# Optimization experiments

Hardware: AMD Instinct MI355X
Metric: run time of the kernel (lower is better)

Reference implementation:

```python
import jax, jax.numpy as jnp
import numpy as np

NUM_STATES = 512
NUM_OBS = 1024
BATCH = 64
T = 512


def setup_inputs() -> dict:
    key = jax.random.key(0)
    k_obs, k_pi, k_A, k_B = jax.random.split(key, 4)
    observations = jax.random.randint(k_obs, (BATCH, T), 0, NUM_OBS, dtype=jnp.int32)
    log_pi = jax.random.normal(k_pi, (NUM_STATES,), dtype=jnp.float32)
    log_A = jax.random.normal(k_A, (NUM_STATES, NUM_STATES), dtype=jnp.float32)
    log_B = jax.random.normal(k_B, (NUM_STATES, NUM_OBS), dtype=jnp.float32)
    return {"observations": observations, "log_pi": log_pi, "log_A": log_A, "log_B": log_B}


def _hmm_loglik(observations, log_pi, log_A, log_B):
    # Normalize parameters in log-space (as in the torch module).
    lpi = jax.nn.log_softmax(log_pi, axis=0)            # (S,)
    lA = jax.nn.log_softmax(log_A, axis=1)              # (S, S)
    lB = jax.nn.log_softmax(log_B, axis=1)              # (S, O)

    # Emission log-probs per timestep: (B, T, S)
    emit = lB.T[observations]                            # gather columns of lB

    alpha0 = lpi[None, :] + emit[:, 0, :]                # (B, S)

    def step(alpha, emit_t):
        # alpha: (B, S) over previous state i; transition lA[i, j]
        alpha_next = jax.scipy.special.logsumexp(alpha[:, :, None] + lA[None, :, :], axis=1) + emit_t
        return alpha_next, None

    # scan over time axis; emit[:, 1:, :] -> (T-1, B, S)
    alpha_T, _ = jax.lax.scan(step, alpha0, jnp.swapaxes(emit[:, 1:, :], 0, 1))
    log_probs = jax.scipy.special.logsumexp(alpha_T, axis=1)  # (B,)
    return log_probs.sum()


def reference(observations, log_pi, log_A, log_B):
    return _hmm_loglik(observations, log_pi, log_A, log_B)
```

## Files before the change

### kernel.cpp

```cpp
#include <hip/hip_runtime.h>

#define S     512
#define NOBS  1024
#define TT    512
#define CH    16
#define NWAVE 8
#define NJT   4
#define NGRP  4

typedef __attribute__((ext_vector_type(4))) float f32x4;
typedef __attribute__((ext_vector_type(4))) int   i32x4;
typedef __attribute__((ext_vector_type(8))) int   i32x8;
typedef __attribute__((ext_vector_type(2))) unsigned int u32x2;
typedef long i64;

__device__ __forceinline__ unsigned short f2bf(float x) {
  unsigned u = __builtin_bit_cast(unsigned, x);
  return (unsigned short)((u + 0x7fffu + ((u >> 16) & 1u)) >> 16);
}
__device__ __forceinline__ float bflo(unsigned u) {
  return __builtin_bit_cast(float, u << 16);
}
__device__ __forceinline__ float bfhi(unsigned u) {
  return __builtin_bit_cast(float, u & 0xffff0000u);
}

__device__ __forceinline__ unsigned char f2fp8_sw(float x) {
  x = fminf(fmaxf(x, 0.f), 448.f);
  unsigned u = __builtin_bit_cast(unsigned, x);
  int ex = (int)((u >> 23) & 0xff);
  if (ex >= 121) {
    unsigned m = (u & 0x7fffff) | 0x800000;
    unsigned keep = m >> 20, rest = m & 0xfffff;
    keep += (rest > 0x80000u) || (rest == 0x80000u && (keep & 1));
    int e8 = ex - 127 + 7;
    if (keep == 16) { keep = 8; e8++; }
    if (e8 >= 16) return 0x7e;
    return (unsigned char)((e8 << 3) | (keep & 7));
  } else {
    int m = (int)(x * 512.0f + 0.5f);
    if (m > 8) m = 8;
    return (unsigned char)m;
  }
}

__device__ __forceinline__ unsigned pack4_fp8(float p0, float p1, float p2, float p3) {
#if __has_builtin(__builtin_amdgcn_cvt_pk_fp8_f32)
  int v = __builtin_amdgcn_cvt_pk_fp8_f32(p0, p1, 0, false);
  v = __builtin_amdgcn_cvt_pk_fp8_f32(p2, p3, v, true);
  return (unsigned)v;
#else
  return (unsigned)f2fp8_sw(p0) | ((unsigned)f2fp8_sw(p1) << 8) |
         ((unsigned)f2fp8_sw(p2) << 16) | ((unsigned)f2fp8_sw(p3) << 24);
#endif
}

__device__ __forceinline__ float wave_max(float v) {
  for (int d = 32; d; d >>= 1) v = fmaxf(v, __shfl_xor(v, d));
  return v;
}
__device__ __forceinline__ float wave_sum(float v) {
  for (int d = 32; d; d >>= 1) v += __shfl_xor(v, d);
  return v;
}

__global__ void prep_pi(const float* __restrict__ log_pi, float* __restrict__ lpi) {
  const int l = threadIdx.x;
  float v[8];
  float mx = -INFINITY;
  for (int k = 0; k < 8; ++k) { v[k] = log_pi[l + 64 * k]; mx = fmaxf(mx, v[k]); }
  mx = wave_max(mx);
  float sm = 0.f;
  for (int k = 0; k < 8; ++k) sm += __expf(v[k] - mx);
  sm = wave_sum(sm);
  const float lse = mx + __logf(sm);
  for (int k = 0; k < 8; ++k) lpi[l + 64 * k] = v[k] - lse;
}

__global__ void prep_B(const float* __restrict__ log_B, unsigned short* __restrict__ Bexp16) {
  const int j = blockIdx.x, l = threadIdx.x;
  const float* row = log_B + (size_t)j * NOBS;
  float v[16];
  float mx = -INFINITY;
  for (int k = 0; k < 16; ++k) { v[k] = row[l + 64 * k]; mx = fmaxf(mx, v[k]); }
  mx = wave_max(mx);
  float sm = 0.f;
  for (int k = 0; k < 16; ++k) sm += __expf(v[k] - mx);
  sm = wave_sum(sm);
  const float lse = mx + __logf(sm);
  for (int k = 0; k < 16; ++k) Bexp16[(size_t)(l + 64 * k) * S + j] = f2bf(__expf(v[k] - lse));
}

__global__ void prep_A(const float* __restrict__ log_A, unsigned char* __restrict__ Afrag8) {
  const int i = blockIdx.x, l = threadIdx.x;
  const float* row = log_A + (size_t)i * S;
  float v[8];
  float mx = -INFINITY;
  for (int k = 0; k < 8; ++k) { v[k] = row[l + 64 * k]; mx = fmaxf(mx, v[k]); }
  mx = wave_max(mx);
  float sm = 0.f;
  for (int k = 0; k < 8; ++k) sm += __expf(v[k] - mx);
  sm = wave_sum(sm);
  const float lse = mx + __logf(sm);
  const int c = i >> 7, g4s = (i >> 5) & 3, e = i & 31;
  for (int k = 0; k < 8; ++k) {
    const int j = l + 64 * k;
    const int jt = j >> 4, jc = j & 15;
    Afrag8[((size_t)(jt * 4 + c) * 64 + g4s * 16 + jc) * 32 + e] = f2fp8_sw(__expf(v[k] - lse));
  }
}

__device__ __forceinline__ int pswz(int m, int g) { return m * 512 + (((g ^ m) & 31) << 4); }

__global__ __launch_bounds__(512, 2)
void hmm_main(const int* __restrict__ obs, const float* __restrict__ lpi,
              const unsigned short* __restrict__ Bexp16,
              const unsigned char* __restrict__ Afrag8, float* __restrict__ parts)
{
  __shared__ __align__(16) unsigned char Pb[CH * S];
  __shared__ int   obs_s[CH][TT];
  __shared__ __align__(16) float pred[CH][NWAVE];

  const int tid = threadIdx.x;
  const int w   = tid >> 6;
  const int l   = tid & 63;
  const int g4  = l >> 4;
  const int mm  = l & 15;
  const int grp = blockIdx.x;

  i32x8 a_frags[NJT][4];
  #pragma unroll
  for (int ji = 0; ji < NJT; ++ji) {
    const int jt = w + NWAVE * ji;
    #pragma unroll
    for (int c = 0; c < 4; ++c)
      a_frags[ji][c] = *reinterpret_cast<const i32x8*>(
          Afrag8 + ((size_t)(jt * 4 + c) * 64 + l) * 32);
  }

  for (int m = 0; m < CH; ++m)
    obs_s[m][tid] = obs[(size_t)(grp * CH + m) * TT + tid];
  __syncthreads();

  float lsc = 0.f;

  for (int t = 0; t < TT; ++t) {
    const bool fin = (t == TT - 1);
    f32x4 vals[NJT];

    if (t == 0) {
      const int o0 = obs_s[mm][0];
      #pragma unroll
      for (int ji = 0; ji < NJT; ++ji) {
        const int j0 = (w + NWAVE * ji) * 16 + g4 * 4;
        const f32x4 lp = *reinterpret_cast<const f32x4*>(lpi + j0);
        const u32x2 e = *reinterpret_cast<const u32x2*>(Bexp16 + (size_t)o0 * S + j0);
        vals[ji][0] = lp[0] + __logf(bflo(e[0]));
        vals[ji][1] = lp[1] + __logf(bfhi(e[0]));
        vals[ji][2] = lp[2] + __logf(bflo(e[1]));
        vals[ji][3] = lp[3] + __logf(bfhi(e[1]));
      }
    } else {
      const int ob = obs_s[mm][t];
      u32x2 eb[NJT];
      const unsigned short* bp = Bexp16 + (size_t)ob * S + g4 * 4;
      #pragma unroll
      for (int ji = 0; ji < NJT; ++ji)
        eb[ji] = *reinterpret_cast<const u32x2*>(bp + (w + NWAVE * ji) * 16);

      i32x8 af[4];
      #pragma unroll
      for (int c = 0; c < 4; ++c) {
        const int g0 = c * 8 + g4 * 2;
        i32x4 lo = *reinterpret_cast<const i32x4*>(&Pb[pswz(mm, g0)]);
        i32x4 hi = *reinterpret_cast<const i32x4*>(&Pb[pswz(mm, g0 + 1)]);
        af[c] = i32x8{lo[0], lo[1], lo[2], lo[3], hi[0], hi[1], hi[2], hi[3]};
      }
      #pragma unroll
      for (int ji = 0; ji < NJT; ++ji) {
        f32x4 acc = {0.f, 0.f, 0.f, 0.f};
        #pragma unroll
        for (int c = 0; c < 4; ++c) {
#if __has_builtin(__builtin_amdgcn_mfma_scale_f32_16x16x128_f8f6f4)
          acc = __builtin_amdgcn_mfma_scale_f32_16x16x128_f8f6f4(
                    a_frags[ji][c], af[c], acc, 0, 0,
                    0, 0x7f7f7f7f, 0, 0x7f7f7f7f);
#else
          const i64* pa = reinterpret_cast<const i64*>(&a_frags[ji][c]);
          const i64* pb = reinterpret_cast<const i64*>(&af[c]);
          #pragma unroll
          for (int q = 0; q < 4; ++q)
            acc = __builtin_amdgcn_mfma_f32_16x16x32_fp8_fp8(pa[q], pb[q], acc, 0, 0, 0);
#endif
        }
        acc[0] *= bflo(eb[ji][0]);
        acc[1] *= bfhi(eb[ji][0]);
        acc[2] *= bflo(eb[ji][1]);
        acc[3] *= bfhi(eb[ji][1]);
        vals[ji] = acc;
      }
    }

    float v;
    if (fin) {
      f32x4 sv = vals[0] + vals[1] + vals[2] + vals[3];
      v = (sv[0] + sv[1]) + (sv[2] + sv[3]);
      v += __shfl_xor(v, 16);
      v += __shfl_xor(v, 32);
    } else {
      f32x4 mv;
      #pragma unroll
      for (int r = 0; r < 4; ++r)
        mv[r] = fmaxf(fmaxf(vals[0][r], vals[1][r]), fmaxf(vals[2][r], vals[3][r]));
      v = fmaxf(fmaxf(mv[0], mv[1]), fmaxf(mv[2], mv[3]));
      v = fmaxf(v, __shfl_xor(v, 16));
      v = fmaxf(v, __shfl_xor(v, 32));
    }
    if (g4 == 0) pred[mm][w] = v;
    __syncthreads();

    if (!fin) {
      const f32x4 p0 = *reinterpret_cast<const f32x4*>(&pred[mm][0]);
      const f32x4 p1 = *reinterpret_cast<const f32x4*>(&pred[mm][4]);
      const float s = fmaxf(fmaxf(fmaxf(p0[0], p0[1]), fmaxf(p0[2], p0[3])),
                            fmaxf(fmaxf(p1[0], p1[1]), fmaxf(p1[2], p1[3])));
      float inv;
      if (t == 0) { lsc = s;           inv = s; }
      else        { lsc += __logf(s);  inv = __builtin_amdgcn_rcpf(s); }

      #pragma unroll
      for (int ji = 0; ji < NJT; ++ji) {
        const int jt = w + NWAVE * ji;
        float q0, q1, q2, q3;
        if (t == 0) {
          q0 = __expf(vals[ji][0] - inv); q1 = __expf(vals[ji][1] - inv);
          q2 = __expf(vals[ji][2] - inv); q3 = __expf(vals[ji][3] - inv);
        } else {
          q0 = vals[ji][0] * inv; q1 = vals[ji][1] * inv;
          q2 = vals[ji][2] * inv; q3 = vals[ji][3] * inv;
        }
        *reinterpret_cast<unsigned*>(&Pb[pswz(mm, jt) + g4 * 4]) = pack4_fp8(q0, q1, q2, q3);
      }
      __syncthreads();
    } else {
      if (w == 0 && g4 == 0) {
        const f32x4 p0 = *reinterpret_cast<const f32x4*>(&pred[mm][0]);
        const f32x4 p1 = *reinterpret_cast<const f32x4*>(&pred[mm][4]);
        const float s8 = ((p0[0] + p0[1]) + (p0[2] + p0[3])) +
                         ((p1[0] + p1[1]) + (p1[2] + p1[3]));
        float cl = lsc + __logf(s8);
        for (int d = 1; d < 16; d <<= 1) cl += __shfl_xor(cl, d);
        if (l == 0) parts[grp] = cl;
      }
    }
  }
}

__global__ void final_sum(const float* __restrict__ parts, float* __restrict__ out) {
  out[0] = parts[0] + parts[1] + parts[2] + parts[3];
}

extern "C" void kernel_launch(void* const* d_in, const int* in_sizes, int n_in,
                              void* d_out, int out_size, void* d_ws, size_t ws_size,
                              hipStream_t stream) {
  const int*   obs  = (const int*)d_in[0];
  const float* lgpi = (const float*)d_in[1];
  const float* lgA  = (const float*)d_in[2];
  const float* lgB  = (const float*)d_in[3];
  float* out = (float*)d_out;

  char* ws = (char*)d_ws;
  unsigned short* Bexp16 = (unsigned short*)ws;
  unsigned char*  Afrag8 = (unsigned char*)(ws + (size_t)NOBS * S * 2);
  float*          lpi    = (float*)(ws + (size_t)NOBS * S * 2 + (size_t)S * S);
  float*          parts  = lpi + S;

  prep_pi<<<1, 64, 0, stream>>>(lgpi, lpi);
  prep_B<<<S, 64, 0, stream>>>(lgB, Bexp16);
  prep_A<<<S, 64, 0, stream>>>(lgA, Afrag8);
  hmm_main<<<NGRP, 512, 0, stream>>>(obs, lpi, Bexp16, Afrag8, parts);
  final_sum<<<1, 1, 0, stream>>>(parts, out);
}
```

Baseline: 841.6 us.

## Double-buffer probability tile and use predicted scale to drop one barrier per step

The per-step loop now uses double-buffered shared-memory probability and max buffers. The normalization scale for step t is predicted from the previous step's max plus a clamped growth-rate extrapolation, so the MFMA results can be scaled and written straight to the next buffer. This cuts the block barriers per timestep from two to one and removes the separate max-then-normalize pass from the critical path. In exchange, values can drift away from unit max within the clamped range, which may cost some FP8 precision.

```diff
diff --git a/kernel.cpp b/kernel.cpp
--- a/kernel.cpp
+++ b/kernel.cpp
@@ -112,20 +112,31 @@
 
 __device__ __forceinline__ int pswz(int m, int g) { return m * 512 + (((g ^ m) & 31) << 4); }
 
+__device__ __forceinline__ float max8(const float* p) {
+  const f32x4 p0 = *reinterpret_cast<const f32x4*>(p);
+  const f32x4 p1 = *reinterpret_cast<const f32x4*>(p + 4);
+  return fmaxf(fmaxf(fmaxf(p0[0], p0[1]), fmaxf(p0[2], p0[3])),
+               fmaxf(fmaxf(p1[0], p1[1]), fmaxf(p1[2], p1[3])));
+}
+__device__ __forceinline__ float sum8(const float* p) {
+  const f32x4 p0 = *reinterpret_cast<const f32x4*>(p);
+  const f32x4 p1 = *reinterpret_cast<const f32x4*>(p + 4);
+  return ((p0[0] + p0[1]) + (p0[2] + p0[3])) + ((p1[0] + p1[1]) + (p1[2] + p1[3]));
+}
+
+#define CLAMP_LN8 2.0794415f
+
 __global__ __launch_bounds__(512, 2)
 void hmm_main(const int* __restrict__ obs, const float* __restrict__ lpi,
               const unsigned short* __restrict__ Bexp16,
               const unsigned char* __restrict__ Afrag8, float* __restrict__ parts)
 {
-  __shared__ __align__(16) unsigned char Pb[CH * S];
-  __shared__ int   obs_s[CH][TT];
-  __shared__ __align__(16) float pred[CH][NWAVE];
+  __shared__ __align__(16) unsigned char Pb[2][CH * S];
+  __shared__ int obs_s[CH][TT + 1];
+  __shared__ __align__(16) float pred[2][CH][12];
 
   const int tid = threadIdx.x;
-  const int w   = tid >> 6;
-  const int l   = tid & 63;
-  const int g4  = l >> 4;
-  const int mm  = l & 15;
+  const int w = tid >> 6, l = tid & 63, g4 = l >> 4, mm = l & 15;
   const int grp = blockIdx.x;
 
   i32x8 a_frags[NJT][4];
@@ -142,116 +153,209 @@
     obs_s[m][tid] = obs[(size_t)(grp * CH + m) * TT + tid];
   __syncthreads();
 
-  float lsc = 0.f;
-
-  for (int t = 0; t < TT; ++t) {
-    const bool fin = (t == TT - 1);
+  float lsc, Lu1, e1;
+
+  {
+    const int o0 = obs_s[mm][0];
     f32x4 vals[NJT];
-
-    if (t == 0) {
-      const int o0 = obs_s[mm][0];
-      #pragma unroll
-      for (int ji = 0; ji < NJT; ++ji) {
-        const int j0 = (w + NWAVE * ji) * 16 + g4 * 4;
-        const f32x4 lp = *reinterpret_cast<const f32x4*>(lpi + j0);
-        const u32x2 e = *reinterpret_cast<const u32x2*>(Bexp16 + (size_t)o0 * S + j0);
-        vals[ji][0] = lp[0] + __logf(bflo(e[0]));
-        vals[ji][1] = lp[1] + __logf(bfhi(e[0]));
-        vals[ji][2] = lp[2] + __logf(bflo(e[1]));
-        vals[ji][3] = lp[3] + __logf(bfhi(e[1]));
-      }
-    } else {
-      const int ob = obs_s[mm][t];
-      u32x2 eb[NJT];
-      const unsigned short* bp = Bexp16 + (size_t)ob * S + g4 * 4;
-      #pragma unroll
-      for (int ji = 0; ji < NJT; ++ji)
-        eb[ji] = *reinterpret_cast<const u32x2*>(bp + (w + NWAVE * ji) * 16);
-
-      i32x8 af[4];
+    #pragma unroll
+    for (int ji = 0; ji < NJT; ++ji) {
+      const int j0 = (w + NWAVE * ji) * 16 + g4 * 4;
+      const f32x4 lp = *reinterpret_cast<const f32x4*>(lpi + j0);
+      const u32x2 e = *reinterpret_cast<const u32x2*>(Bexp16 + (size_t)o0 * S + j0);
+      vals[ji][0] = lp[0] + __logf(bflo(e[0]));
+      vals[ji][1] = lp[1] + __logf(bfhi(e[0]));
+      vals[ji][2] = lp[2] + __logf(bflo(e[1]));
+      vals[ji][3] = lp[3] + __logf(bfhi(e[1]));
+    }
+    float v = -INFINITY;
+    #pragma unroll
+    for (int ji = 0; ji < NJT; ++ji)
+      v = fmaxf(v, fmaxf(fmaxf(vals[ji][0], vals[ji][1]), fmaxf(vals[ji][2], vals[ji][3])));
+    v = fmaxf(v, __shfl_xor(v, 16));
+    v = fmaxf(v, __shfl_xor(v, 32));
+    if (g4 == 0) pred[0][mm][w] = v;
+    __syncthreads();
+    const float M0 = max8(&pred[0][mm][0]);
+    #pragma unroll
+    for (int ji = 0; ji < NJT; ++ji) {
+      const int jt = w + NWAVE * ji;
+      *reinterpret_cast<unsigned*>(&Pb[0][pswz(mm, jt) + g4 * 4]) =
+          pack4_fp8(__expf(vals[ji][0] - M0), __expf(vals[ji][1] - M0),
+                    __expf(vals[ji][2] - M0), __expf(vals[ji][3] - M0));
+    }
+    lsc = M0;
+    __syncthreads();
+  }
+
+  {
+    const int o1 = obs_s[mm][1];
+    u32x2 eb[NJT];
+    const unsigned short* bp = Bexp16 + (size_t)o1 * S + g4 * 4;
+    #pragma unroll
+    for (int ji = 0; ji < NJT; ++ji)
+      eb[ji] = *reinterpret_cast<const u32x2*>(bp + (w + NWAVE * ji) * 16);
+    i32x8 af[4];
+    #pragma unroll
+    for (int c = 0; c < 4; ++c) {
+      const int g0 = c * 8 + g4 * 2;
+      i32x4 lo = *reinterpret_cast<const i32x4*>(&Pb[0][pswz(mm, g0)]);
+      i32x4 hi = *reinterpret_cast<const i32x4*>(&Pb[0][pswz(mm, g0 + 1)]);
+      af[c] = i32x8{lo[0], lo[1], lo[2], lo[3], hi[0], hi[1], hi[2], hi[3]};
+    }
+    f32x4 vals[NJT];
+    #pragma unroll
+    for (int ji = 0; ji < NJT; ++ji) {
+      f32x4 acc = {0.f, 0.f, 0.f, 0.f};
       #pragma unroll
       for (int c = 0; c < 4; ++c) {
-        const int g0 = c * 8 + g4 * 2;
-        i32x4 lo = *reinterpret_cast<const i32x4*>(&Pb[pswz(mm, g0)]);
-        i32x4 hi = *reinterpret_cast<const i32x4*>(&Pb[pswz(mm, g0 + 1)]);
-        af[c] = i32x8{lo[0], lo[1], lo[2], lo[3], hi[0], hi[1], hi[2], hi[3]};
+#if __has_builtin(__builtin_amdgcn_mfma_scale_f32_16x16x128_f8f6f4)
+        acc = __builtin_amdgcn_mfma_scale_f32_16x16x128_f8f6f4(
+                  a_frags[ji][c], af[c], acc, 0, 0, 0, 0x7f7f7f7f, 0, 0x7f7f7f7f);
+#else
+        const i64* pa = reinterpret_cast<const i64*>(&a_frags[ji][c]);
+        const i64* pb = reinterpret_cast<const i64*>(&af[c]);
+        #pragma unroll
+        for (int q = 0; q < 4; ++q)
+          acc = __builtin_amdgcn_mfma_f32_16x16x32_fp8_fp8(pa[q], pb[q], acc, 0, 0, 0);
+#endif
       }
+      acc[0] *= bflo(eb[ji][0]); acc[1] *= bfhi(eb[ji][0]);
+      acc[2] *= bflo(eb[ji][1]); acc[3] *= bfhi(eb[ji][1]);
+      vals[ji] = acc;
+    }
+    float v = -INFINITY;
+    #pragma unroll
+    for (int ji = 0; ji < NJT; ++ji)
+      v = fmaxf(v, fmaxf(fmaxf(vals[ji][0], vals[ji][1]), fmaxf(vals[ji][2], vals[ji][3])));
+    v = fmaxf(v, __shfl_xor(v, 16));
+    v = fmaxf(v, __shfl_xor(v, 32));
+    if (g4 == 0) pred[1][mm][w] = v;
+    __syncthreads();
+    const float v1 = max8(&pred[1][mm][0]);
+    const float inv = __builtin_amdgcn_rcpf(v1);
+    Lu1 = __logf(v1); lsc += Lu1; e1 = 0.f;
+    #pragma unroll
+    for (int ji = 0; ji < NJT; ++ji) {
+      const int jt = w + NWAVE * ji;
+      *reinterpret_cast<unsigned*>(&Pb[1][pswz(mm, jt) + g4 * 4]) =
+          pack4_fp8(vals[ji][0] * inv, vals[ji][1] * inv,
+                    vals[ji][2] * inv, vals[ji][3] * inv);
+    }
+    __syncthreads();
+  }
+
+  for (int t = 2; t < TT - 1; ++t) {
+    const int cur = t & 1, prv = cur ^ 1;
+    const int ob = obs_s[mm][t];
+
+    const float pm = max8(&pred[prv][mm][0]);
+    float e_new = (t == 2) ? 0.f : __logf(pm);
+
+    u32x2 eb[NJT];
+    const unsigned short* bp = Bexp16 + (size_t)ob * S + g4 * 4;
+    #pragma unroll
+    for (int ji = 0; ji < NJT; ++ji)
+      eb[ji] = *reinterpret_cast<const u32x2*>(bp + (w + NWAVE * ji) * 16);
+
+    i32x8 af[4];
+    #pragma unroll
+    for (int c = 0; c < 4; ++c) {
+      const int g0 = c * 8 + g4 * 2;
+      i32x4 lo = *reinterpret_cast<const i32x4*>(&Pb[prv][pswz(mm, g0)]);
+      i32x4 hi = *reinterpret_cast<const i32x4*>(&Pb[prv][pswz(mm, g0 + 1)]);
+      af[c] = i32x8{lo[0], lo[1], lo[2], lo[3], hi[0], hi[1], hi[2], hi[3]};
+    }
+
+    const float dr = fminf(fmaxf(e_new - e1, -CLAMP_LN8), CLAMP_LN8);
+    const float Lu = Lu1 + e_new + dr;
+    const float inv = __expf(-Lu);
+    lsc += Lu; e1 = e_new; Lu1 = Lu;
+
+    float vmax = 0.f;
+    #pragma unroll
+    for (int ji = 0; ji < NJT; ++ji) {
+      f32x4 acc = {0.f, 0.f, 0.f, 0.f};
       #pragma unroll
-      for (int ji = 0; ji < NJT; ++ji) {
-        f32x4 acc = {0.f, 0.f, 0.f, 0.f};
+      for (int c = 0; c < 4; ++c) {
+#if __has_builtin(__builtin_amdgcn_mfma_scale_f32_16x16x128_f8f6f4)
+        acc = __builtin_amdgcn_mfma_scale_f32_16x16x128_f8f6f4(
+                  a_frags[ji][c], af[c], acc, 0, 0, 0, 0x7f7f7f7f, 0, 0x7f7f7f7f);
+#else
+        const i64* pa = reinterpret_cast<const i64*>(&a_frags[ji][c]);
+        const i64* pb = reinterpret_cast<const i64*>(&af[c]);
         #pragma unroll
-        for (int c = 0; c < 4; ++c) {
+        for (int q = 0; q < 4; ++q)
+          acc = __builtin_amdgcn_mfma_f32_16x16x32_fp8_fp8(pa[q], pb[q], acc, 0, 0, 0);
+#endif
+      }
+      const float q0 = acc[0] * bflo(eb[ji][0]) * inv;
+      const float q1 = acc[1] * bfhi(eb[ji][0]) * inv;
+      const float q2 = acc[2] * bflo(eb[ji][1]) * inv;
+      const float q3 = acc[3] * bfhi(eb[ji][1]) * inv;
+      const int jt = w + NWAVE * ji;
+      *reinterpret_cast<unsigned*>(&Pb[cur][pswz(mm, jt) + g4 * 4]) =
+          pack4_fp8(q0, q1, q2, q3);
+      vmax = fmaxf(vmax, fmaxf(fmaxf(q0, q1), fmaxf(q2, q3)));
+    }
+    vmax = fmaxf(vmax, __shfl_xor(vmax, 16));
+    vmax = fmaxf(vmax, __shfl_xor(vmax, 32));
+    if (g4 == 0) pred[cur][mm][w] = vmax;
+    __syncthreads();
+  }
+
+  {
+    const int t = TT - 1, cur = t & 1, prv = cur ^ 1;
+    const int ob = obs_s[mm][t];
+    const float pm = max8(&pred[prv][mm][0]);
+    const float e_new = __logf(pm);
+    u32x2 eb[NJT];
+    const unsigned short* bp = Bexp16 + (size_t)ob * S + g4 * 4;
+    #pragma unroll
+    for (int ji = 0; ji < NJT; ++ji)
+      eb[ji] = *reinterpret_cast<const u32x2*>(bp + (w + NWAVE * ji) * 16);
+    i32x8 af[4];
+    #pragma unroll
+    for (int c = 0; c < 4; ++c) {
+      const int g0 = c * 8 + g4 * 2;
+      i32x4 lo = *reinterpret_cast<const i32x4*>(&Pb[prv][pswz(mm, g0)]);
+      i32x4 hi = *reinterpret_cast<const i32x4*>(&Pb[prv][pswz(mm, g0 + 1)]);
+      af[c] = i32x8{lo[0], lo[1], lo[2], lo[3], hi[0], hi[1], hi[2], hi[3]};
+    }
+    const float dr = fminf(fmaxf(e_new - e1, -CLAMP_LN8), CLAMP_LN8);
+    const float Lu = Lu1 + e_new + dr;
+    const float inv = __expf(-Lu);
+    lsc += Lu;
+    float ssum = 0.f;
+    #pragma unroll
+    for (int ji = 0; ji < NJT; ++ji) {
+      f32x4 acc = {0.f, 0.f, 0.f, 0.f};
+      #pragma unroll
+      for (int c = 0; c < 4; ++c) {
 #if __has_builtin(__builtin_amdgcn_mfma_scale_f32_16x16x128_f8f6f4)
-          acc = __builtin_amdgcn_mfma_scale_f32_16x16x128_f8f6f4(
-                    a_frags[ji][c], af[c], acc, 0, 0,
-                    0, 0x7f7f7f7f, 0, 0x7f7f7f7f);
+        acc = __builtin_amdgcn_mfma_scale_f32_16x16x128_f8f6f4(
+                  a_frags[ji][c], af[c], acc, 0, 0, 0, 0x7f7f7f7f, 0, 0x7f7f7f7f);
 #else
-          const i64* pa = reinterpret_cast<const i64*>(&a_frags[ji][c]);
-          const i64* pb = reinterpret_cast<const i64*>(&af[c]);
-          #pragma unroll
-          for (int q = 0; q < 4; ++q)
-            acc = __builtin_amdgcn_mfma_f32_16x16x32_fp8_fp8(pa[q], pb[q], acc, 0, 0, 0);
+        const i64* pa = reinterpret_cast<const i64*>(&a_frags[ji][c]);
+        const i64* pb = reinterpret_cast<const i64*>(&af[c]);
+        #pragma unroll
+        for (int q = 0; q < 4; ++q)
+          acc = __builtin_amdgcn_mfma_f32_16x16x32_fp8_fp8(pa[q], pb[q], acc, 0, 0, 0);
 #endif
-        }
-        acc[0] *= bflo(eb[ji][0]);
-        acc[1] *= bfhi(eb[ji][0]);
-        acc[2] *= bflo(eb[ji][1]);
-        acc[3] *= bfhi(eb[ji][1]);
-        vals[ji] = acc;
       }
-    }
-
-    float v;
-    if (fin) {
-      f32x4 sv = vals[0] + vals[1] + vals[2] + vals[3];
-      v = (sv[0] + sv[1]) + (sv[2] + sv[3]);
-      v += __shfl_xor(v, 16);
-      v += __shfl_xor(v, 32);
-    } else {
-      f32x4 mv;
-      #pragma unroll
-      for (int r = 0; r < 4; ++r)
-        mv[r] = fmaxf(fmaxf(vals[0][r], vals[1][r]), fmaxf(vals[2][r], vals[3][r]));
-      v = fmaxf(fmaxf(mv[0], mv[1]), fmaxf(mv[2], mv[3]));
-      v = fmaxf(v, __shfl_xor(v, 16));
-      v = fmaxf(v, __shfl_xor(v, 32));
-    }
-    if (g4 == 0) pred[mm][w] = v;
-    __syncthreads();
-
-    if (!fin) {
-      const f32x4 p0 = *reinterpret_cast<const f32x4*>(&pred[mm][0]);
-      const f32x4 p1 = *reinterpret_cast<const f32x4*>(&pred[mm][4]);
-      const float s = fmaxf(fmaxf(fmaxf(p0[0], p0[1]), fmaxf(p0[2], p0[3])),
-                            fmaxf(fmaxf(p1[0], p1[1]), fmaxf(p1[2], p1[3])));
-      float inv;
-      if (t == 0) { lsc = s;           inv = s; }
-      else        { lsc += __logf(s);  inv = __builtin_amdgcn_rcpf(s); }
-
-      #pragma unroll
-      for (int ji = 0; ji < NJT; ++ji) {
-        const int jt = w + NWAVE * ji;
-        float q0, q1, q2, q3;
-        if (t == 0) {
-          q0 = __expf(vals[ji][0] - inv); q1 = __expf(vals[ji][1] - inv);
-          q2 = __expf(vals[ji][2] - inv); q3 = __expf(vals[ji][3] - inv);
-        } else {
-          q0 = vals[ji][0] * inv; q1 = vals[ji][1] * inv;
-          q2 = vals[ji][2] * inv; q3 = vals[ji][3] * inv;
-        }
-        *reinterpret_cast<unsigned*>(&Pb[pswz(mm, jt) + g4 * 4]) = pack4_fp8(q0, q1, q2, q3);
-      }
-      __syncthreads();
-    } else {
-      if (w == 0 && g4 == 0) {
-        const f32x4 p0 = *reinterpret_cast<const f32x4*>(&pred[mm][0]);
-        const f32x4 p1 = *reinterpret_cast<const f32x4*>(&pred[mm][4]);
-        const float s8 = ((p0[0] + p0[1]) + (p0[2] + p0[3])) +
-                         ((p1[0] + p1[1]) + (p1[2] + p1[3]));
-        float cl = lsc + __logf(s8);
-        for (int d = 1; d < 16; d <<= 1) cl += __shfl_xor(cl, d);
-        if (l == 0) parts[grp] = cl;
-      }
+      ssum += acc[0] * bflo(eb[ji][0]) + acc[1] * bfhi(eb[ji][0]) +
+              acc[2] * bflo(eb[ji][1]) + acc[3] * bfhi(eb[ji][1]);
+    }
+    ssum *= inv;
+    ssum += __shfl_xor(ssum, 16);
+    ssum += __shfl_xor(ssum, 32);
+    if (g4 == 0) pred[cur][mm][w] = ssum;
+    __syncthreads();
+    if (w == 0 && g4 == 0) {
+      const float s8 = sum8(&pred[1][mm][0]);
+      float cl = lsc + __logf(s8);
+      for (int d = 1; d < 16; d <<= 1) cl += __shfl_xor(cl, d);
+      if (l == 0) parts[grp] = cl;
     }
   }
 }
```

Measured after the change: 716.1 us. -14.9%, faster.
